# Kernel tuning notes

Measured on AMD Instinct MI355X. Metric: run time of the kernel, lower is better.

## Reference

```python
import jax, jax.numpy as jnp
import numpy as np

Z = 128      # z_size
N = 256      # n_neurons_param_net
F = 2048     # n_functions
B = 8192     # batch


def setup_inputs() -> dict:
    key = jax.random.key(0)
    ks = jax.random.split(key, 16)
    sN = 1.0 / np.sqrt(N)
    inp = {
        "t": jax.random.uniform(ks[0], (1,), dtype=jnp.float32),
        "z_and_logpz": jax.random.normal(ks[1], (B, Z + 1), dtype=jnp.float32),
        # stacked first two layers of the 4 parameter-predicting MLPs
        # order: [w_in_net, w_out_net, b_net, gate_net]
        "W1": jax.random.normal(ks[2], (4, N, 1), dtype=jnp.float32),
        "B1": jax.random.normal(ks[3], (4, N), dtype=jnp.float32) * 0.01,
        "W2": jax.random.normal(ks[4], (4, N, N), dtype=jnp.float32) * sN,
        "B2": jax.random.normal(ks[5], (4, N), dtype=jnp.float32) * 0.01,
        # per-head final layers
        "W3_win": jax.random.normal(ks[6], (F * Z, N), dtype=jnp.float32) * sN,
        "b3_win": jax.random.normal(ks[7], (F * Z,), dtype=jnp.float32) * 0.01,
        "W3_wout": jax.random.normal(ks[8], (F * Z, N), dtype=jnp.float32) * sN,
        "b3_wout": jax.random.normal(ks[9], (F * Z,), dtype=jnp.float32) * 0.01,
        "W3_b": jax.random.normal(ks[10], (F, N), dtype=jnp.float32) * sN,
        "b3_b": jax.random.normal(ks[11], (F,), dtype=jnp.float32) * 0.01,
        "W3_gate": jax.random.normal(ks[12], (F, N), dtype=jnp.float32) * sN,
        "b3_gate": jax.random.normal(ks[13], (F,), dtype=jnp.float32) * 0.01,
    }
    return inp


def reference(t, z_and_logpz, W1, B1, W2, B2, W3_win, b3_win,
              W3_wout, b3_wout, W3_b, b3_b, W3_gate, b3_gate):
    F_ = W3_b.shape[0]
    Z_ = W3_win.shape[0] // F_
    ts = t.reshape(())  # scalar time

    # parameter-predicting MLPs (4 tiny 3-layer MLPs, first 2 layers stacked)
    h0 = jnp.tanh(W1[:, :, 0] * ts + B1)                    # [4, N]
    h1 = jnp.tanh(jnp.einsum('knm,km->kn', W2, h0) + B2)    # [4, N]
    w_in = (W3_win @ h1[0] + b3_win).reshape(F_, Z_)        # [F, Z]
    w_out = (W3_wout @ h1[1] + b3_wout).reshape(F_, Z_)     # [F, Z]
    b = W3_b @ h1[2] + b3_b                                 # [F]
    gate = jax.nn.sigmoid(W3_gate @ h1[3] + b3_gate)        # [F]

    z = z_and_logpz[:, :Z_]                                 # [B, Z]
    h = jnp.tanh(z @ w_in.T + b)                            # [B, F]
    g = h * gate                                            # gated hidden
    dz_dt = (g @ w_out) / F_                                # mean over functions -> [B, Z]

    # exact Jacobian trace (analytic; identical to autograd trace of this net):
    # d f_i / d z_i = mean_f gate_f * (1 - h_f^2) * w_out[f,i] * w_in[f,i]
    s = jnp.sum(w_in * w_out, axis=1)                       # [F]
    trace = ((1.0 - h * h) * gate) @ s / F_                 # [B]
    dlogpz_dt = -trace[:, None]                             # [B, 1]
    return jnp.concatenate([dz_dt, dlogpz_dt], axis=-1)     # [B, Z+1]
```

## Files before the change

### kernel.cpp

```cpp
#include <hip/hip_runtime.h>
#include <hip/hip_bf16.h>
#include <math.h>

typedef float f32x4 __attribute__((ext_vector_type(4)));
typedef float f32x4u __attribute__((ext_vector_type(4))) __attribute__((aligned(4)));
typedef short s16x8 __attribute__((ext_vector_type(8)));

__device__ __forceinline__ float wave_reduce64(float v) {
#pragma unroll
    for (int m = 32; m > 0; m >>= 1) v += __shfl_xor(v, m, 64);
    return v;
}

__device__ __forceinline__ unsigned short f32_to_bf16_rn(float x) {
    unsigned int u = __float_as_uint(x);
    unsigned int r = (u + 0x7fffu + ((u >> 16) & 1u)) >> 16;
    return (unsigned short)r;
}
__device__ __forceinline__ float bf16_to_f32(unsigned short h) {
    return __uint_as_float(((unsigned int)h) << 16);
}

__global__ __launch_bounds__(256) void kA(const float* __restrict__ t,
                                          const float* __restrict__ W1, const float* __restrict__ B1,
                                          const float* __restrict__ W2, const float* __restrict__ B2,
                                          float* __restrict__ h1) {
    const int tid = threadIdx.x;
    const int wave = (blockIdx.x << 2) + (tid >> 6);
    const int lane = tid & 63;
    const int k = wave >> 8, n = wave & 255;
    const float ts = t[0];
    const int m0 = lane << 2;
    f32x4 w1 = *(const f32x4*)(W1 + k * 256 + m0);
    f32x4 b1 = *(const f32x4*)(B1 + k * 256 + m0);
    f32x4 w2 = *(const f32x4*)(W2 + (size_t)(k * 256 + n) * 256 + m0);
    float p = 0.f;
    p += w2.x * tanhf(w1.x * ts + b1.x);
    p += w2.y * tanhf(w1.y * ts + b1.y);
    p += w2.z * tanhf(w1.z * ts + b1.z);
    p += w2.w * tanhf(w1.w * ts + b1.w);
    p = wave_reduce64(p);
    if (lane == 0) h1[k * 256 + n] = tanhf(p + B2[k * 256 + n]);
}

__global__ __launch_bounds__(256) void kB(const float* __restrict__ Wwin, const float* __restrict__ bwin,
                                          const float* __restrict__ Wwout, const float* __restrict__ bwout,
                                          const float* __restrict__ Wb, const float* __restrict__ bb,
                                          const float* __restrict__ Wg, const float* __restrict__ bg,
                                          const float* __restrict__ h1,
                                          float* __restrict__ w_in, float* __restrict__ w_out,
                                          unsigned short* __restrict__ w_in_hi, unsigned short* __restrict__ w_in_lo,
                                          unsigned short* __restrict__ w_out_t,
                                          float* __restrict__ b_arr, float* __restrict__ gate) {
    const int lane = threadIdx.x & 63;
    const int wave0 = (blockIdx.x << 2) + (threadIdx.x >> 6);
    const int nwaves = gridDim.x << 2;
    const int m0 = lane << 2;
    const f32x4 h_win  = *(const f32x4*)(h1 + m0);
    const f32x4 h_wout = *(const f32x4*)(h1 + 256 + m0);
    const f32x4 h_b    = *(const f32x4*)(h1 + 512 + m0);
    const f32x4 h_g    = *(const f32x4*)(h1 + 768 + m0);
    for (int g = wave0; g < 132096; g += nwaves) {
        const int r = g << 2;
        const float* W; const float* bias; f32x4 hv; int idx, seg;
        if (r < 262144)      { seg = 0; idx = r;          W = Wwin;  bias = bwin;  hv = h_win; }
        else if (r < 524288) { seg = 1; idx = r - 262144; W = Wwout; bias = bwout; hv = h_wout; }
        else if (r < 526336) { seg = 2; idx = r - 524288; W = Wb;    bias = bb;    hv = h_b; }
        else                 { seg = 3; idx = r - 526336; W = Wg;    bias = bg;    hv = h_g; }
        const float* base = W + (size_t)idx * 256 + m0;
        f32x4 w0 = *(const f32x4*)(base);
        f32x4 w1 = *(const f32x4*)(base + 256);
        f32x4 w2 = *(const f32x4*)(base + 512);
        f32x4 w3 = *(const f32x4*)(base + 768);
        float p0 = w0.x * hv.x + w0.y * hv.y + w0.z * hv.z + w0.w * hv.w;
        float p1 = w1.x * hv.x + w1.y * hv.y + w1.z * hv.z + w1.w * hv.w;
        float p2 = w2.x * hv.x + w2.y * hv.y + w2.z * hv.z + w2.w * hv.w;
        float p3 = w3.x * hv.x + w3.y * hv.y + w3.z * hv.z + w3.w * hv.w;
#pragma unroll
        for (int m = 32; m > 0; m >>= 1) {
            p0 += __shfl_xor(p0, m, 64);
            p1 += __shfl_xor(p1, m, 64);
            p2 += __shfl_xor(p2, m, 64);
            p3 += __shfl_xor(p3, m, 64);
        }
        if (lane < 4) {
            float v = (lane == 0) ? p0 : (lane == 1) ? p1 : (lane == 2) ? p2 : p3;
            const int id2 = idx + lane;
            v += bias[id2];
            if (seg == 0) {
                w_in[id2] = v;
                unsigned short hi = f32_to_bf16_rn(v);
                w_in_hi[id2] = hi;
                w_in_lo[id2] = f32_to_bf16_rn(v - bf16_to_f32(hi));
            } else if (seg == 1) {
                w_out[id2] = v;
                w_out_t[(size_t)(id2 & 127) * 2048 + (id2 >> 7)] = f32_to_bf16_rn(v);
            } else if (seg == 2) {
                b_arr[id2] = v;
            } else {
                gate[id2] = 1.f / (1.f + __expf(-v));
            }
        }
    }
}

__global__ __launch_bounds__(256) void kC(const float* __restrict__ w_in, const float* __restrict__ w_out,
                                          float* __restrict__ s) {
    const int f = (blockIdx.x << 2) + (threadIdx.x >> 6);
    const int lane = threadIdx.x & 63;
    float2 a = *(const float2*)(w_in + (size_t)f * 128 + lane * 2);
    float2 b = *(const float2*)(w_out + (size_t)f * 128 + lane * 2);
    float p = a.x * b.x + a.y * b.y;
    p = wave_reduce64(p);
    if (lane == 0) s[f] = p;
}

__global__ __launch_bounds__(256) void kD(const float* __restrict__ zin,
                                          const unsigned short* __restrict__ w_in_hi,
                                          const unsigned short* __restrict__ w_in_lo,
                                          const unsigned short* __restrict__ w_out_t,
                                          const float* __restrict__ b_arr, const float* __restrict__ gate,
                                          const float* __restrict__ s, float* __restrict__ out) {
    __shared__ __attribute__((aligned(16))) unsigned short g_lds[4][16][72];
    __shared__ __attribute__((aligned(16))) float red[3][64][36];

    const int tid = threadIdx.x;
    const int w = tid >> 6, lane = tid & 63;
    const int q = lane >> 4, lm = lane & 15;
    const int b0 = blockIdx.x * 16;
    const int brow = b0 + lm;

    s16x8 zh[4], zl[4];
#pragma unroll
    for (int kt = 0; kt < 4; kt++) {
        const float* zp = zin + (size_t)brow * 129 + kt * 32 + q * 8;
        f32x4u z0 = *(const f32x4u*)(zp);
        f32x4u z1 = *(const f32x4u*)(zp + 4);
        float zv[8] = {z0.x, z0.y, z0.z, z0.w, z1.x, z1.y, z1.z, z1.w};
#pragma unroll
        for (int j = 0; j < 8; j++) {
            unsigned short hi = f32_to_bf16_rn(zv[j]);
            zh[kt][j] = (short)hi;
            zl[kt][j] = (short)f32_to_bf16_rn(zv[j] - bf16_to_f32(hi));
        }
    }

    f32x4 acc2[8];
#pragma unroll
    for (int ct = 0; ct < 8; ct++) acc2[ct] = (f32x4){0.f, 0.f, 0.f, 0.f};
    float tr[4] = {0.f, 0.f, 0.f, 0.f};

    for (int ch = 0; ch < 8; ch++) {
        const int f0 = w * 512 + ch * 64;
#pragma unroll
        for (int nt = 0; nt < 4; nt++) {
            const int fc = f0 + nt * 16 + lm;
            const unsigned short* ph = w_in_hi + (size_t)fc * 128;
            const unsigned short* pl = w_in_lo + (size_t)fc * 128;
            f32x4 acc1 = {0.f, 0.f, 0.f, 0.f};
#pragma unroll
            for (int kt = 0; kt < 4; kt++) {
                s16x8 bh = *(const s16x8*)(ph + kt * 32 + q * 8);
                s16x8 bl = *(const s16x8*)(pl + kt * 32 + q * 8);
                acc1 = __builtin_amdgcn_mfma_f32_16x16x32_bf16(zh[kt], bh, acc1, 0, 0, 0);
                acc1 = __builtin_amdgcn_mfma_f32_16x16x32_bf16(zh[kt], bl, acc1, 0, 0, 0);
                acc1 = __builtin_amdgcn_mfma_f32_16x16x32_bf16(zl[kt], bh, acc1, 0, 0, 0);
            }
            const float gv = gate[fc], bv = b_arr[fc], sv = s[fc];
#pragma unroll
            for (int i = 0; i < 4; i++) {
                float pre = acc1[i] + bv;
                float e = __expf(2.f * pre);
                float th = 1.f - 2.f * __builtin_amdgcn_rcpf(e + 1.f);
                float g = th * gv;
                tr[i] += (1.f - th * th) * gv * sv;
                g_lds[w][q * 4 + i][nt * 16 + lm] = f32_to_bf16_rn(g);
            }
        }
#pragma unroll
        for (int kt2 = 0; kt2 < 2; kt2++) {
            s16x8 af = *(const s16x8*)&g_lds[w][lm][kt2 * 32 + q * 8];
#pragma unroll
            for (int ct = 0; ct < 8; ct++) {
                s16x8 bf = *(const s16x8*)(w_out_t + (size_t)(ct * 16 + lm) * 2048 + f0 + kt2 * 32 + q * 8);
                acc2[ct] = __builtin_amdgcn_mfma_f32_16x16x32_bf16(af, bf, acc2[ct], 0, 0, 0);
            }
        }
    }

    if (w != 0) {
#pragma unroll
        for (int ct = 0; ct < 8; ct++) *(f32x4*)&red[w - 1][lane][ct * 4] = acc2[ct];
        *(f32x4*)&red[w - 1][lane][32] = (f32x4){tr[0], tr[1], tr[2], tr[3]};
    }
    __syncthreads();
    if (w == 0) {
#pragma unroll
        for (int ww = 0; ww < 3; ww++) {
#pragma unroll
            for (int ct = 0; ct < 8; ct++) {
                f32x4 o = *(const f32x4*)&red[ww][lane][ct * 4];
                acc2[ct].x += o.x; acc2[ct].y += o.y; acc2[ct].z += o.z; acc2[ct].w += o.w;
            }
            f32x4 to = *(const f32x4*)&red[ww][lane][32];
            tr[0] += to.x; tr[1] += to.y; tr[2] += to.z; tr[3] += to.w;
        }

        const float inv = 1.f / 2048.f;
#pragma unroll
        for (int ct = 0; ct < 8; ct++)
#pragma unroll
            for (int i = 0; i < 4; i++)
                out[(size_t)(b0 + q * 4 + i) * 129 + ct * 16 + lm] = acc2[ct][i] * inv;
#pragma unroll
        for (int i = 0; i < 4; i++) {
            float t2 = tr[i];
            t2 += __shfl_xor(t2, 1, 64);
            t2 += __shfl_xor(t2, 2, 64);
            t2 += __shfl_xor(t2, 4, 64);
            t2 += __shfl_xor(t2, 8, 64);
            if (lm == 0) out[(size_t)(b0 + q * 4 + i) * 129 + 128] = -t2 * inv;
        }
    }
}

extern "C" void kernel_launch(void* const* d_in, const int* in_sizes, int n_in,
                              void* d_out, int out_size, void* d_ws, size_t ws_size,
                              hipStream_t stream) {
    const float* t     = (const float*)d_in[0];
    const float* z     = (const float*)d_in[1];
    const float* W1    = (const float*)d_in[2];
    const float* B1    = (const float*)d_in[3];
    const float* W2    = (const float*)d_in[4];
    const float* B2    = (const float*)d_in[5];
    const float* W3win = (const float*)d_in[6];
    const float* b3win = (const float*)d_in[7];
    const float* W3wo  = (const float*)d_in[8];
    const float* b3wo  = (const float*)d_in[9];
    const float* W3b   = (const float*)d_in[10];
    const float* b3b   = (const float*)d_in[11];
    const float* W3g   = (const float*)d_in[12];
    const float* b3g   = (const float*)d_in[13];
    float* out = (float*)d_out;

    float* h1    = (float*)d_ws;
    float* w_in  = h1 + 1024;
    float* w_out = w_in + 262144;
    float* b_arr = w_out + 262144;
    float* gate  = b_arr + 2048;
    float* s     = gate + 2048;
    unsigned short* w_in_hi = (unsigned short*)(s + 2048);
    unsigned short* w_in_lo = w_in_hi + 262144;
    unsigned short* w_out_t = w_in_lo + 262144;

    kA<<<256, 256, 0, stream>>>(t, W1, B1, W2, B2, h1);
    kB<<<2048, 256, 0, stream>>>(W3win, b3win, W3wo, b3wo, W3b, b3b, W3g, b3g, h1,
                                 w_in, w_out, w_in_hi, w_in_lo, w_out_t, b_arr, gate);
    kC<<<512, 256, 0, stream>>>(w_in, w_out, s);
    kD<<<512, 256, 0, stream>>>(z, w_in_hi, w_in_lo, w_out_t, b_arr, gate, s, out);
    (void)in_sizes; (void)n_in; (void)out_size; (void)ws_size;
}
```

Baseline: 635.0 us.

## Stream final-layer weights into LDS via async global_load_lds double buffering

Replaces the final-layer GEMV kernel with a persistent 256-block version that copies 64-row weight chunks straight into padded LDS with global_load_lds, double-buffered with a prefetch distance of two chunks. Each block computes dot products from LDS while the next chunk is in flight, aiming to keep HBM streaming of the large W3 matrices saturated. The previous kernel is kept as a fallback if the large dynamic LDS size cannot be set. The cost is heavy LDS use per block, which limits occupancy to one block per CU, plus manual vmcnt/lgkmcnt waits that must match the DMA count exactly.

Result: no change. 624.0 us (-1.7%).

```diff
diff --git a/kernel.cpp b/kernel.cpp
--- a/kernel.cpp
+++ b/kernel.cpp
@@ -19,6 +19,13 @@
 }
 __device__ __forceinline__ float bf16_to_f32(unsigned short h) {
     return __uint_as_float(((unsigned int)h) << 16);
+}
+
+__device__ __forceinline__ void dma_row16(const float* gsrc, float* ldst) {
+    __builtin_amdgcn_global_load_lds(
+        (const __attribute__((address_space(1))) unsigned int*)gsrc,
+        (__attribute__((address_space(3))) unsigned int*)ldst,
+        16, 0, 0);
 }
 
 __global__ __launch_bounds__(256) void kA(const float* __restrict__ t,
@@ -43,15 +50,121 @@
     if (lane == 0) h1[k * 256 + n] = tanhf(p + B2[k * 256 + n]);
 }
 
-__global__ __launch_bounds__(256) void kB(const float* __restrict__ Wwin, const float* __restrict__ bwin,
-                                          const float* __restrict__ Wwout, const float* __restrict__ bwout,
-                                          const float* __restrict__ Wb, const float* __restrict__ bb,
-                                          const float* __restrict__ Wg, const float* __restrict__ bg,
-                                          const float* __restrict__ h1,
-                                          float* __restrict__ w_in, float* __restrict__ w_out,
-                                          unsigned short* __restrict__ w_in_hi, unsigned short* __restrict__ w_in_lo,
-                                          unsigned short* __restrict__ w_out_t,
-                                          float* __restrict__ b_arr, float* __restrict__ gate) {
+__global__ __launch_bounds__(256) void kB_dma(const float* __restrict__ Wwin, const float* __restrict__ bwin,
+                                              const float* __restrict__ Wwout, const float* __restrict__ bwout,
+                                              const float* __restrict__ Wb, const float* __restrict__ bb,
+                                              const float* __restrict__ Wg, const float* __restrict__ bg,
+                                              const float* __restrict__ h1,
+                                              float* __restrict__ w_in, float* __restrict__ w_out,
+                                              unsigned short* __restrict__ w_in_hi, unsigned short* __restrict__ w_in_lo,
+                                              unsigned short* __restrict__ w_out_t,
+                                              float* __restrict__ b_arr, float* __restrict__ gate) {
+    extern __shared__ float smem[];
+    float* h_s = smem;
+    float* bufs = smem + 1088;
+
+    const int tid = threadIdx.x;
+    const int w = tid >> 6, lane = tid & 63;
+
+    {
+        const int seg = tid >> 6, q = (tid >> 4) & 3, i = tid & 15;
+        f32x4 hv = *(const f32x4*)(h1 + seg * 256 + q * 64 + i * 4);
+        *(f32x4*)(h_s + seg * 272 + q * 68 + i * 4) = hv;
+    }
+
+    const int r = lane >> 2, c = lane & 3;
+
+#pragma unroll
+    for (int pk = 0; pk < 2; pk++) {
+        const int ci = blockIdx.x + pk * 256;
+        const float* W; int row0;
+        if (ci < 4096)      { W = Wwin;  row0 = ci * 64; }
+        else if (ci < 8192) { W = Wwout; row0 = (ci - 4096) * 64; }
+        else if (ci < 8224) { W = Wb;    row0 = (ci - 8192) * 64; }
+        else                { W = Wg;    row0 = (ci - 8224) * 64; }
+        const float* src = W + (size_t)(row0 + w * 16) * 256 + (lane << 2);
+        float* dst = bufs + (size_t)((pk * 4 + w) * 16) * 260;
+#pragma unroll
+        for (int rr = 0; rr < 16; rr++) dma_row16(src + rr * 256, dst + rr * 260);
+    }
+
+    __syncthreads();
+
+    for (int k = 0;; k++) {
+        const int cur = blockIdx.x + k * 256;
+        if (cur >= 8256) break;
+        const int buf = k & 1;
+        const bool has_next = (cur + 256) < 8256;
+        if (has_next) asm volatile("s_waitcnt vmcnt(16)" ::: "memory");
+        else          asm volatile("s_waitcnt vmcnt(0)" ::: "memory");
+
+        int seg, row0;
+        const float* bias;
+        if (cur < 4096)      { seg = 0; row0 = cur * 64;          bias = bwin; }
+        else if (cur < 8192) { seg = 1; row0 = (cur - 4096) * 64; bias = bwout; }
+        else if (cur < 8224) { seg = 2; row0 = (cur - 8192) * 64; bias = bb; }
+        else                 { seg = 3; row0 = (cur - 8224) * 64; bias = bg; }
+
+        const float* rowp = bufs + (size_t)((buf * 4 + w) * 16 + r) * 260 + c * 64;
+        const float* hp = h_s + seg * 272 + c * 68;
+        float a0 = 0.f, a1 = 0.f;
+#pragma unroll
+        for (int j = 0; j < 16; j += 2) {
+            f32x4 d0 = *(const f32x4*)(rowp + 4 * j);
+            f32x4 h0 = *(const f32x4*)(hp + 4 * j);
+            f32x4 d1 = *(const f32x4*)(rowp + 4 * j + 4);
+            f32x4 h1v = *(const f32x4*)(hp + 4 * j + 4);
+            a0 += d0.x * h0.x + d0.y * h0.y + d0.z * h0.z + d0.w * h0.w;
+            a1 += d1.x * h1v.x + d1.y * h1v.y + d1.z * h1v.z + d1.w * h1v.w;
+        }
+        float acc = a0 + a1;
+        acc += __shfl_xor(acc, 1, 64);
+        acc += __shfl_xor(acc, 2, 64);
+
+        if (c == 0) {
+            const int idx = row0 + w * 16 + r;
+            float v = acc + bias[idx];
+            if (seg == 0) {
+                w_in[idx] = v;
+                unsigned short hi = f32_to_bf16_rn(v);
+                w_in_hi[idx] = hi;
+                w_in_lo[idx] = f32_to_bf16_rn(v - bf16_to_f32(hi));
+            } else if (seg == 1) {
+                w_out[idx] = v;
+                w_out_t[(size_t)(idx & 127) * 2048 + (idx >> 7)] = f32_to_bf16_rn(v);
+            } else if (seg == 2) {
+                b_arr[idx] = v;
+            } else {
+                gate[idx] = 1.f / (1.f + __expf(-v));
+            }
+        }
+
+        asm volatile("s_waitcnt lgkmcnt(0)" ::: "memory");
+
+        const int pf = cur + 512;
+        if (pf < 8256) {
+            const float* W; int prow0;
+            if (pf < 4096)      { W = Wwin;  prow0 = pf * 64; }
+            else if (pf < 8192) { W = Wwout; prow0 = (pf - 4096) * 64; }
+            else if (pf < 8224) { W = Wb;    prow0 = (pf - 8192) * 64; }
+            else                { W = Wg;    prow0 = (pf - 8224) * 64; }
+            const float* src = W + (size_t)(prow0 + w * 16) * 256 + (lane << 2);
+            float* dst = bufs + (size_t)((buf * 4 + w) * 16) * 260;
+#pragma unroll
+            for (int rr = 0; rr < 16; rr++) dma_row16(src + rr * 256, dst + rr * 260);
+        }
+    }
+}
+
+__global__ __launch_bounds__(256) void kB_fb(const float* __restrict__ Wwin, const float* __restrict__ bwin,
+                                             const float* __restrict__ Wwout, const float* __restrict__ bwout,
+                                             const float* __restrict__ Wb, const float* __restrict__ bb,
+                                             const float* __restrict__ Wg, const float* __restrict__ bg,
+                                             const float* __restrict__ h1,
+                                             float* __restrict__ w_in, float* __restrict__ w_out,
+                                             unsigned short* __restrict__ w_in_hi, unsigned short* __restrict__ w_in_lo,
+                                             unsigned short* __restrict__ w_out_t,
+                                             float* __restrict__ b_arr, float* __restrict__ gate) {
     const int lane = threadIdx.x & 63;
     const int wave0 = (blockIdx.x << 2) + (threadIdx.x >> 6);
     const int nwaves = gridDim.x << 2;
@@ -61,12 +174,12 @@
     const f32x4 h_b    = *(const f32x4*)(h1 + 512 + m0);
     const f32x4 h_g    = *(const f32x4*)(h1 + 768 + m0);
     for (int g = wave0; g < 132096; g += nwaves) {
-        const int r = g << 2;
+        const int rr = g << 2;
         const float* W; const float* bias; f32x4 hv; int idx, seg;
-        if (r < 262144)      { seg = 0; idx = r;          W = Wwin;  bias = bwin;  hv = h_win; }
-        else if (r < 524288) { seg = 1; idx = r - 262144; W = Wwout; bias = bwout; hv = h_wout; }
-        else if (r < 526336) { seg = 2; idx = r - 524288; W = Wb;    bias = bb;    hv = h_b; }
-        else                 { seg = 3; idx = r - 526336; W = Wg;    bias = bg;    hv = h_g; }
+        if (rr < 262144)      { seg = 0; idx = rr;          W = Wwin;  bias = bwin;  hv = h_win; }
+        else if (rr < 524288) { seg = 1; idx = rr - 262144; W = Wwout; bias = bwout; hv = h_wout; }
+        else if (rr < 526336) { seg = 2; idx = rr - 524288; W = Wb;    bias = bb;    hv = h_b; }
+        else                  { seg = 3; idx = rr - 526336; W = Wg;    bias = bg;    hv = h_g; }
         const float* base = W + (size_t)idx * 256 + m0;
         f32x4 w0 = *(const f32x4*)(base);
         f32x4 w1 = *(const f32x4*)(base + 256);
@@ -254,8 +367,17 @@
     unsigned short* w_out_t = w_in_lo + 262144;
 
     kA<<<256, 256, 0, stream>>>(t, W1, B1, W2, B2, h1);
-    kB<<<2048, 256, 0, stream>>>(W3win, b3win, W3wo, b3wo, W3b, b3b, W3g, b3g, h1,
-                                 w_in, w_out, w_in_hi, w_in_lo, w_out_t, b_arr, gate);
+
+    const int kb_lds = (1088 + 8 * 16 * 260) * 4;
+    hipError_t attr_ok = hipFuncSetAttribute((const void*)kB_dma,
+                                             hipFuncAttributeMaxDynamicSharedMemorySize, kb_lds);
+    if (attr_ok == hipSuccess) {
+        kB_dma<<<256, 256, kb_lds, stream>>>(W3win, b3win, W3wo, b3wo, W3b, b3b, W3g, b3g, h1,
+                                             w_in, w_out, w_in_hi, w_in_lo, w_out_t, b_arr, gate);
+    } else {
+        kB_fb<<<2048, 256, 0, stream>>>(W3win, b3win, W3wo, b3wo, W3b, b3b, W3g, b3g, h1,
+                                        w_in, w_out, w_in_hi, w_in_lo, w_out_t, b_arr, gate);
+    }
     kC<<<512, 256, 0, stream>>>(w_in, w_out, s);
     kD<<<512, 256, 0, stream>>>(z, w_in_hi, w_in_lo, w_out_t, b_arr, gate, s, out);
     (void)in_sizes; (void)n_in; (void)out_size; (void)ws_size;
```
